# Kernel tuning notes

Measured on AMD Instinct MI355X. Metric: run time of the kernel, lower is better.

The kernel has to match this reference:

```python
import jax, jax.numpy as jnp
import numpy as np

B, S, D, F = 32, 512, 1024, 4096
R_COMMON, R_DOMAIN, E = 16, 16, 8
ALPHA = 2.0


def setup_inputs() -> dict:
    key = jax.random.key(0)
    ks = jax.random.split(key, 12)
    sd = lambda k, shape: jax.random.normal(k, shape, dtype=jnp.float32) * (1.0 / np.sqrt(shape[-1]))
    return {
        "hidden_states": jax.random.normal(ks[0], (B, S, D), dtype=jnp.float32),
        "expert_ids": jax.random.randint(ks[1], (B,), 0, E, dtype=jnp.int32),
        # nn.Linear weights: [out_features, in_features]
        "wi": sd(ks[2], (F, D)),
        "wo": sd(ks[3], (D, F)),
        "common_wi_a": sd(ks[4], (R_COMMON, D)),
        "common_wi_b": sd(ks[5], (F, R_COMMON)),
        "common_wo_a": sd(ks[6], (R_COMMON, F)),
        "common_wo_b": sd(ks[7], (D, R_COMMON)),
        # stacked per-expert LoRA weights
        "experts_wi_a": sd(ks[8], (E, R_DOMAIN, D)),
        "experts_wi_b": sd(ks[9], (F, R_DOMAIN)) * jnp.ones((E, 1, 1)) * 0.0 + sd(ks[9], (E, F, R_DOMAIN)),
        "experts_wo_a": sd(ks[10], (E, R_DOMAIN, F)),
        "experts_wo_b": sd(ks[11], (E, D, R_DOMAIN)),
    }


def _expert_lora(x, expert_ids, Wa, Wb):
    """Per-row (dim 0) expert LoRA correction, vectorized via gather.

    x: [B, S, din]; Wa: [E, r, din]; Wb: [E, dout, r].
    Equivalent to the per-expert mask-gather/scatter-add loop since each
    row belongs to exactly one expert.
    """
    Ab = Wa[expert_ids]  # [B, r, din]
    Bb = Wb[expert_ids]  # [B, dout, r]
    low = jnp.einsum("bsd,brd->bsr", x, Ab)
    return ALPHA * jnp.einsum("bsr,bor->bso", low, Bb)


def reference(hidden_states, expert_ids, wi, wo,
              common_wi_a, common_wi_b, common_wo_a, common_wo_b,
              experts_wi_a, experts_wi_b, experts_wo_a, experts_wo_b):
    x = hidden_states
    hidden_i = jnp.einsum("bsd,fd->bsf", x, wi)
    hidden_i += ALPHA * jnp.einsum("bsr,fr->bsf", jnp.einsum("bsd,rd->bsr", x, common_wi_a), common_wi_b)
    hidden_i += _expert_lora(x, expert_ids, experts_wi_a, experts_wi_b)
    hidden_i = jax.nn.relu(hidden_i)  # dense_act_fn='relu'; dropout is identity (eval)
    hidden_o = jnp.einsum("bsf,df->bsd", hidden_i, wo)
    hidden_o += ALPHA * jnp.einsum("bsr,dr->bsd", jnp.einsum("bsf,rf->bsr", hidden_i, common_wo_a), common_wo_b)
    hidden_o += _expert_lora(hidden_i, expert_ids, experts_wo_a, experts_wo_b)
    return hidden_o
```

## Files before the change

### kernel.cpp

```cpp
#include <hip/hip_runtime.h>
#include <hip/hip_bf16.h>
#include <stdint.h>

#define B_ 32
#define S_ 512
#define D_ 1024
#define F_ 4096
#define N_ (B_*S_)
#define E_ 8
#define ALPHA_ 2.0f

#define LDA1 1088
#define LDA2 4160

typedef __hip_bfloat16 bf16;
typedef __attribute__((ext_vector_type(8))) short short8;
typedef __attribute__((ext_vector_type(8))) __bf16 bf16x8;
typedef __attribute__((ext_vector_type(4))) float f32x4;

__device__ __forceinline__ f32x4 mfma_bf16(short8 a, short8 b, f32x4 c) {
    return __builtin_amdgcn_mfma_f32_16x16x32_bf16(
        __builtin_bit_cast(bf16x8, a), __builtin_bit_cast(bf16x8, b), c, 0, 0, 0);
}

__device__ __forceinline__ void gload_lds16(const void* g, void* l) {
    __builtin_amdgcn_global_load_lds((const __attribute__((address_space(1))) void*)g,
                                     (__attribute__((address_space(3))) void*)l, 16, 0, 0);
}

__device__ __forceinline__ unsigned pack2(float a, float b) {
    unsigned short x = __builtin_bit_cast(unsigned short, __float2bfloat16(a));
    unsigned short y = __builtin_bit_cast(unsigned short, __float2bfloat16(b));
    return (unsigned)x | ((unsigned)y << 16);
}
__device__ __forceinline__ uint2 pack4(float4 v) {
    return make_uint2(pack2(v.x, v.y), pack2(v.z, v.w));
}

__global__ __launch_bounds__(256) void prep_w_kernel(
    const float* __restrict__ wi, const float* __restrict__ wo,
    const float* __restrict__ cwia, const float* __restrict__ cwib,
    const float* __restrict__ cwoa, const float* __restrict__ cwob,
    const float* __restrict__ ewia, const float* __restrict__ ewib,
    const float* __restrict__ ewoa, const float* __restrict__ ewob,
    bf16* __restrict__ wi_b, bf16* __restrict__ wo_b,
    bf16* __restrict__ ex1, bf16* __restrict__ ex2,
    bf16* __restrict__ wilo, bf16* __restrict__ wolo)
{
    const int tid0 = blockIdx.x * blockDim.x + threadIdx.x;
    const int stride = gridDim.x * blockDim.x;

    for (int i = tid0; i < F_*D_/4; i += stride) {
        ((uint2*)wi_b)[i] = pack4(((const float4*)wi)[i]);
        ((uint2*)wo_b)[i] = pack4(((const float4*)wo)[i]);
    }
    for (int i = tid0; i < E_*F_*16; i += stride) {
        int e = i >> 16; int rem = i & 0xFFFF; int f = rem >> 4; int r = rem & 15;
        bf16* dst = ex1 + (((size_t)e*F_ + f) << 6);
        dst[r]      = __float2bfloat16(cwib[f*16 + r]);
        dst[16 + r] = __float2bfloat16(ewib[(((size_t)e*F_ + f) << 4) + r]);
        dst[32 + r] = __float2bfloat16(0.f);
        dst[48 + r] = __float2bfloat16(0.f);
    }
    for (int i = tid0; i < E_*D_*16; i += stride) {
        int e = i >> 14; int rem = i & 0x3FFF; int d = rem >> 4; int r = rem & 15;
        bf16* dst = ex2 + (((size_t)e*D_ + d) << 6);
        dst[r]      = __float2bfloat16(cwob[d*16 + r]);
        dst[16 + r] = __float2bfloat16(ewob[(((size_t)e*D_ + d) << 4) + r]);
        dst[32 + r] = __float2bfloat16(0.f);
        dst[48 + r] = __float2bfloat16(0.f);
    }
    for (int i = tid0; i < E_*32*(D_/4); i += stride) {
        int e = i / (32*(D_/4)); int rem = i - e*(32*(D_/4));
        int r = rem / (D_/4); int c4 = (rem % (D_/4)) * 4;
        const float* src = (r < 16) ? (cwia + (size_t)r*D_ + c4)
                                    : (ewia + ((size_t)(e*16 + (r-16)))*D_ + c4);
        *(uint2*)(wilo + ((size_t)(e*32 + r))*D_ + c4) = pack4(*(const float4*)src);
    }
    for (int i = tid0; i < E_*32*(F_/4); i += stride) {
        int e = i / (32*(F_/4)); int rem = i - e*(32*(F_/4));
        int r = rem / (F_/4); int c4 = (rem % (F_/4)) * 4;
        const float* src = (r < 16) ? (cwoa + (size_t)r*F_ + c4)
                                    : (ewoa + ((size_t)(e*16 + (r-16)))*F_ + c4);
        *(uint2*)(wolo + ((size_t)(e*32 + r))*F_ + c4) = pack4(*(const float4*)src);
    }
}

__global__ __launch_bounds__(256) void prep_x_kernel(
    const float* __restrict__ x, bf16* __restrict__ A1)
{
    const int tid0 = blockIdx.x * blockDim.x + threadIdx.x;
    const int stride = gridDim.x * blockDim.x;
    for (int i = tid0; i < N_*(D_/4); i += stride) {
        int row = i >> 8; int c4 = (i & 255) << 2;
        float4 v = *(const float4*)(x + (size_t)i * 4);
        *(uint2*)(A1 + (size_t)row*LDA1 + c4) = pack4(v);
    }
    for (int i = tid0; i < N_*8; i += stride) {
        int row = i >> 3; int c = (i & 7) << 2;
        *(uint2*)(A1 + (size_t)row*LDA1 + 1056 + c) = make_uint2(0u, 0u);
    }
}

template<int K>
__global__ __launch_bounds__(256) void lowproj_kernel(
    const bf16* __restrict__ A, const bf16* __restrict__ W,
    const int* __restrict__ eids, bf16* __restrict__ Out,
    int lda, int kout)
{
    constexpr int BM = 64, BK = 64;
    __shared__ __align__(16) bf16 Asm[BM*BK];
    __shared__ __align__(16) bf16 Wsm[32*BK];

    const int tid = threadIdx.x;
    const int row0 = blockIdx.x * BM;
    const int e = eids[row0 >> 9];
    const int w = tid >> 6, lane = tid & 63;
    const int tr = tid >> 3, ts = tid & 7;
    const int lrow = lane & 15;
    const int lk16 = (lane >> 4) << 4;

    f32x4 acc[2] = {};

    int aoff, woff[2];
    { int r = w*16 + lrow; aoff = r*128 + (lk16 ^ ((r & 7) << 4)); }
    #pragma unroll
    for (int n = 0; n < 2; ++n) {
        int r = n*16 + lrow; woff[n] = r*128 + (lk16 ^ ((r & 7) << 4));
    }
    const bf16* Wp = W + (size_t)e * 32 * K;

    #pragma unroll 1
    for (int kt = 0; kt < K/BK; ++kt) {
        const int k0 = kt * BK;
        #pragma unroll
        for (int i = 0; i < 2; ++i) {
            int row = tr + 32*i;
            int slot = ts ^ (row & 7);
            gload_lds16(A + (size_t)(row0 + row)*lda + k0 + slot*8,
                        (char*)Asm + row*128 + ts*16);
        }
        {
            int row = tr;
            int slot = ts ^ (row & 7);
            gload_lds16(Wp + (size_t)row*K + k0 + slot*8,
                        (char*)Wsm + row*128 + ts*16);
        }
        __syncthreads();
        #pragma unroll
        for (int kk = 0; kk < 2; ++kk) {
            short8 a = *(const short8*)((const char*)Asm + (aoff ^ (kk << 6)));
            #pragma unroll
            for (int n = 0; n < 2; ++n) {
                short8 b = *(const short8*)((const char*)Wsm + (woff[n] ^ (kk << 6)));
                acc[n] = mfma_bf16(a, b, acc[n]);
            }
        }
        __syncthreads();
    }

    const int jrow = (lane >> 4) << 2;
    #pragma unroll
    for (int n = 0; n < 2; ++n) {
        #pragma unroll
        for (int j = 0; j < 4; ++j) {
            int r = row0 + w*16 + jrow + j;
            int c = n*16 + lrow;
            Out[(size_t)r*lda + kout + c] = __float2bfloat16(ALPHA_ * acc[n][j]);
        }
    }
    #pragma unroll
    for (int i = 0; i < 8; ++i) {
        int idx = tid*8 + i;
        int r = idx >> 5, c = idx & 31;
        Out[(size_t)(row0 + r)*lda + kout + 32 + c] = __float2bfloat16(0.f);
    }
}

#define DSREAD(base, off) (*(const short8*)((const char*)(base) + (off)))

#define STAGE4(gptr, ld, ldsbase)                                          \
    _Pragma("unroll")                                                      \
    for (int i_ = 0; i_ < 4; ++i_) {                                       \
        int row_ = tr + 64*i_;                                             \
        int slot_ = ts ^ (row_ & 7);                                       \
        gload_lds16((gptr) + (size_t)row_*(ld) + slot_*8,                  \
                    (char*)(ldsbase) + row_*128 + ts*16);                  \
    }

#define STAGE_TILE(KTN, AL, BL)                                            \
  { STAGE4(Ag + (size_t)(KTN)*64, LDAe, AL);                               \
    if ((KTN) < KMAIN_EL/64) { STAGE4(Bg + (size_t)(KTN)*64, LDBe, BL); }  \
    else                     { STAGE4(Bxg, 64, BL); } }

#define TILE_BODY(AC, BC, DOSTAGE, AN, BN, KTN)                            \
  {                                                                        \
             \
    if (DOSTAGE) { STAGE_TILE((KTN), AN, BN); }                            \
    short8 af[4][2]; short8 bq[4][2];                                      \
                                     \
    _Pragma("unroll") for (int m = 0; m < 4; ++m)                          \
      _Pragma("unroll") for (int kk = 0; kk < 2; ++kk)                     \
        af[m][kk] = DSREAD(AC, aoff[m] ^ (kk << 6));                       \
    _Pragma("unroll") for (int n = 0; n < 2; ++n)                          \
      _Pragma("unroll") for (int kk = 0; kk < 2; ++kk)                     \
        bq[n][kk] = DSREAD(BC, boff[n] ^ (kk << 6));                       \
    __builtin_amdgcn_s_setprio(1);                                         \
    _Pragma("unroll") for (int m = 0; m < 4; ++m)                          \
      _Pragma("unroll") for (int n = 0; n < 2; ++n)                        \
        _Pragma("unroll") for (int kk = 0; kk < 2; ++kk)                   \
          acc[m][n] = mfma_bf16(af[m][kk], bq[n][kk], acc[m][n]);          \
    __builtin_amdgcn_s_setprio(0);                                         \
                                                   \
    _Pragma("unroll") for (int n = 2; n < 4; ++n)                          \
      _Pragma("unroll") for (int kk = 0; kk < 2; ++kk)                     \
        bq[n][kk] = DSREAD(BC, boff[n] ^ (kk << 6));                       \
    __builtin_amdgcn_s_setprio(1);                                         \
    _Pragma("unroll") for (int m = 0; m < 4; ++m)                          \
      _Pragma("unroll") for (int n = 2; n < 4; ++n)                        \
        _Pragma("unroll") for (int kk = 0; kk < 2; ++kk)                   \
          acc[m][n] = mfma_bf16(af[m][kk], bq[n][kk], acc[m][n]);          \
    __builtin_amdgcn_s_setprio(0);                                         \
                                              \
    _Pragma("unroll") for (int m = 0; m < 4; ++m)                          \
      _Pragma("unroll") for (int kk = 0; kk < 2; ++kk)                     \
        af[m][kk] = DSREAD(AC, aoff[m+4] ^ (kk << 6));                     \
    __builtin_amdgcn_s_setprio(1);                                         \
    _Pragma("unroll") for (int m = 0; m < 4; ++m)                          \
      _Pragma("unroll") for (int n = 0; n < 2; ++n)                        \
        _Pragma("unroll") for (int kk = 0; kk < 2; ++kk)                   \
          acc[m+4][n] = mfma_bf16(af[m][kk], bq[n][kk], acc[m+4][n]);      \
    __builtin_amdgcn_s_setprio(0);                                         \
                                                             \
    __builtin_amdgcn_s_setprio(1);                                         \
    _Pragma("unroll") for (int m = 0; m < 4; ++m)                          \
      _Pragma("unroll") for (int n = 2; n < 4; ++n)                        \
        _Pragma("unroll") for (int kk = 0; kk < 2; ++kk)                   \
          acc[m+4][n] = mfma_bf16(af[m][kk], bq[n][kk], acc[m+4][n]);      \
    __builtin_amdgcn_s_setprio(0);                                         \
    __syncthreads();                                                       \
  }

template<int KMAIN_EL, int LDAe, int LDBe, int LDCe, int NCOLSe, bool RELU_BF16>
__global__ __launch_bounds__(512, 2) void gemm256_kernel(
    const bf16* __restrict__ A, const bf16* __restrict__ Bmain,
    const bf16* __restrict__ Bextra, const int* __restrict__ eids,
    void* __restrict__ C)
{
    constexpr int MT = N_/256;
    constexpr int NT = NCOLSe/256;
    constexpr int NWG = MT*NT;
    constexpr int KTILES = KMAIN_EL/64 + 1;
    static_assert((KTILES & 1) == 1, "pair loop + tail assumes odd KTILES");
    static_assert(NWG % 8 == 0, "xcd swizzle needs nwg%8==0");
    constexpr int CPX = NWG/8;

    __shared__ __align__(16) bf16 As[2][256*64];
    __shared__ __align__(16) bf16 Bs[2][256*64];

    const int bid = blockIdx.x;
    const int wg = (bid & 7) * CPX + (bid >> 3);
    const int mt = wg % MT, nt = wg / MT;
    const int arow0 = mt * 256, bcol0 = nt * 256;
    const int e = eids[arow0 >> 9];

    const int tid = threadIdx.x;
    const int lane = tid & 63;
    const int wid = tid >> 6;
    const int wm = wid >> 2, wn = wid & 3;
    const int tr = tid >> 3, ts = tid & 7;

    const bf16* Ag  = A + (size_t)arow0 * LDAe;
    const bf16* Bg  = Bmain + (size_t)bcol0 * LDBe;
    const bf16* Bxg = Bextra + ((size_t)e * NCOLSe + bcol0) * 64;

    int aoff[8], boff[4];
    const int lk16 = (lane >> 4) << 4;
    #pragma unroll
    for (int m = 0; m < 8; ++m) {
        int r = wm*128 + m*16 + (lane & 15);
        aoff[m] = r*128 + (lk16 ^ ((r & 7) << 4));
    }
    #pragma unroll
    for (int n = 0; n < 4; ++n) {
        int r = wn*64 + n*16 + (lane & 15);
        boff[n] = r*128 + (lk16 ^ ((r & 7) << 4));
    }

    f32x4 acc[8][4] = {};

    STAGE_TILE(0, As[0], Bs[0]);
    __syncthreads();

    #pragma unroll 1
    for (int t = 0; t < KTILES - 1; t += 2) {
        TILE_BODY(As[0], Bs[0], true, As[1], Bs[1], t + 1);
        TILE_BODY(As[1], Bs[1], true, As[0], Bs[0], t + 2);
    }
    TILE_BODY(As[0], Bs[0], false, As[1], Bs[1], 0);

    const int jrow = (lane >> 4) << 2;
    if constexpr (RELU_BF16) {
        bf16* Cb = (bf16*)C;
        #pragma unroll
        for (int m = 0; m < 8; ++m)
            #pragma unroll
            for (int j = 0; j < 4; ++j) {
                size_t rbase = (size_t)(arow0 + wm*128 + m*16 + jrow + j) * LDCe;
                #pragma unroll
                for (int n = 0; n < 4; ++n) {
                    float v = acc[m][n][j];
                    v = v > 0.f ? v : 0.f;
                    Cb[rbase + bcol0 + wn*64 + n*16 + (lane & 15)] = __float2bfloat16(v);
                }
            }
    } else {
        float* Cf = (float*)C;
        #pragma unroll
        for (int m = 0; m < 8; ++m)
            #pragma unroll
            for (int j = 0; j < 4; ++j) {
                size_t rbase = (size_t)(arow0 + wm*128 + m*16 + jrow + j) * LDCe;
                #pragma unroll
                for (int n = 0; n < 4; ++n)
                    Cf[rbase + bcol0 + wn*64 + n*16 + (lane & 15)] = acc[m][n][j];
            }
    }
}

extern "C" void kernel_launch(void* const* d_in, const int* in_sizes, int n_in,
                              void* d_out, int out_size, void* d_ws, size_t ws_size,
                              hipStream_t stream)
{
    const float* x    = (const float*)d_in[0];
    const int*   eids = (const int*)d_in[1];
    const float* wi   = (const float*)d_in[2];
    const float* wo   = (const float*)d_in[3];
    const float* cwia = (const float*)d_in[4];
    const float* cwib = (const float*)d_in[5];
    const float* cwoa = (const float*)d_in[6];
    const float* cwob = (const float*)d_in[7];
    const float* ewia = (const float*)d_in[8];
    const float* ewib = (const float*)d_in[9];
    const float* ewoa = (const float*)d_in[10];
    const float* ewob = (const float*)d_in[11];

    char* p = (char*)d_ws;
    bf16* A1   = (bf16*)p; p += (size_t)N_*LDA1*sizeof(bf16);
    bf16* A2   = (bf16*)p; p += (size_t)N_*LDA2*sizeof(bf16);
    bf16* wi_b = (bf16*)p; p += (size_t)F_*D_*sizeof(bf16);
    bf16* wo_b = (bf16*)p; p += (size_t)D_*F_*sizeof(bf16);
    bf16* ex1  = (bf16*)p; p += (size_t)E_*F_*64*sizeof(bf16);
    bf16* ex2  = (bf16*)p; p += (size_t)E_*D_*64*sizeof(bf16);
    bf16* wilo = (bf16*)p; p += (size_t)E_*32*D_*sizeof(bf16);
    bf16* wolo = (bf16*)p; p += (size_t)E_*32*F_*sizeof(bf16);

    prep_w_kernel<<<dim3(512), dim3(256), 0, stream>>>(
        wi, wo, cwia, cwib, cwoa, cwob, ewia, ewib, ewoa, ewob,
        wi_b, wo_b, ex1, ex2, wilo, wolo);

    prep_x_kernel<<<dim3(2048), dim3(256), 0, stream>>>(x, A1);

    lowproj_kernel<D_><<<dim3(N_/64), dim3(256), 0, stream>>>(
        A1, wilo, eids, A1, LDA1, D_);

    gemm256_kernel<D_, LDA1, D_, LDA2, F_, true>
        <<<dim3((N_/256)*(F_/256)), dim3(512), 0, stream>>>(A1, wi_b, ex1, eids, A2);

    lowproj_kernel<F_><<<dim3(N_/64), dim3(256), 0, stream>>>(
        A2, wolo, eids, A2, LDA2, F_);

    gemm256_kernel<F_, LDA2, F_, D_, D_, false>
        <<<dim3((N_/256)*(D_/256)), dim3(512), 0, stream>>>(A2, wo_b, ex2, eids, d_out);

    (void)in_sizes; (void)n_in; (void)out_size; (void)ws_size;
}
```

Baseline: 529.1 us.

## Split tile staging into halves interleaved with MFMA phases using partial vmcnt waits

Restructures the double-buffered GEMM main loop so global-to-LDS loads for the next tile are issued in quarter chunks between MFMA groups. Full __syncthreads is replaced with raw s_barrier plus explicit s_waitcnt vmcnt(N) so loads stay in flight across barriers. The goal is to spread memory issue across the tile and avoid a full drain each iteration. It relies on hand-counted vmcnt values and on barrier placement being correct for the LDS buffer reuse, so a miscount risks data races.

```diff
diff --git a/kernel.cpp b/kernel.cpp
--- a/kernel.cpp
+++ b/kernel.cpp
@@ -178,67 +178,73 @@
 }
 
 #define DSREAD(base, off) (*(const short8*)((const char*)(base) + (off)))
-
-#define STAGE4(gptr, ld, ldsbase)                                          \
-    _Pragma("unroll")                                                      \
-    for (int i_ = 0; i_ < 4; ++i_) {                                       \
-        int row_ = tr + 64*i_;                                             \
-        int slot_ = ts ^ (row_ & 7);                                       \
-        gload_lds16((gptr) + (size_t)row_*(ld) + slot_*8,                  \
-                    (char*)(ldsbase) + row_*128 + ts*16);                  \
-    }
-
-#define STAGE_TILE(KTN, AL, BL)                                            \
-  { STAGE4(Ag + (size_t)(KTN)*64, LDAe, AL);                               \
-    if ((KTN) < KMAIN_EL/64) { STAGE4(Bg + (size_t)(KTN)*64, LDBe, BL); }  \
-    else                     { STAGE4(Bxg, 64, BL); } }
-
-#define TILE_BODY(AC, BC, DOSTAGE, AN, BN, KTN)                            \
+#define VMW4 asm volatile("s_waitcnt vmcnt(4)" ::: "memory")
+#define VMW2 asm volatile("s_waitcnt vmcnt(2)" ::: "memory")
+#define VMW0 asm volatile("s_waitcnt vmcnt(0)" ::: "memory")
+#define VMNONE (void)0
+#define BAR __builtin_amdgcn_s_barrier()
+
+#define STAGE_A_HALF(KTN, AL, h)                                           \
+  { const bf16* gpA_ = Ag + (size_t)(KTN)*64;                              \
+    int rA_ = tr + 64*(h);                                                 \
+    int sA_ = ts ^ (rA_ & 7);                                              \
+    gload_lds16(gpA_ + (size_t)rA_*LDAe + sA_*8,                           \
+                (char*)(AL) + rA_*128 + ts*16);                            \
+    int rA2_ = rA_ + 128;                                                  \
+    gload_lds16(gpA_ + (size_t)rA2_*LDAe + sA_*8,                          \
+                (char*)(AL) + rA2_*128 + ts*16); }
+
+#define STAGE_B_HALF(KTN, BL, h)                                           \
+  { const bf16* gpB_; int bldB_; int bkB_;                                 \
+    if ((KTN) < KMAIN_EL/64) { gpB_ = Bg; bldB_ = LDBe; bkB_ = (KTN)*64; } \
+    else                     { gpB_ = Bxg; bldB_ = 64; bkB_ = 0; }         \
+    int rB_ = (tr & 31) + 64*(tr >> 5) + 32*(h);                           \
+    int sB_ = ts ^ (rB_ & 7);                                              \
+    gload_lds16(gpB_ + (size_t)rB_*bldB_ + bkB_ + sB_*8,                   \
+                (char*)(BL) + rB_*128 + ts*16);                            \
+    int rB2_ = rB_ + 128;                                                  \
+    gload_lds16(gpB_ + (size_t)rB2_*bldB_ + bkB_ + sB_*8,                  \
+                (char*)(BL) + rB2_*128 + ts*16); }
+
+#define RD_AF(dst, AC, base)                                               \
+  _Pragma("unroll") for (int m_ = 0; m_ < 4; ++m_)                         \
+    _Pragma("unroll") for (int k_ = 0; k_ < 2; ++k_)                       \
+      dst[m_][k_] = DSREAD(AC, aoff[(base)+m_] ^ (k_ << 6));
+
+#define RD_BQ(dst, BC, base)                                               \
+  _Pragma("unroll") for (int n_ = 0; n_ < 2; ++n_)                         \
+    _Pragma("unroll") for (int k_ = 0; k_ < 2; ++k_)                       \
+      dst[n_][k_] = DSREAD(BC, boff[(base)+n_] ^ (k_ << 6));
+
+#define MFMA16(afr, bqr, mb, nb)                                           \
+  __builtin_amdgcn_s_setprio(1);                                           \
+  _Pragma("unroll") for (int m_ = 0; m_ < 4; ++m_)                         \
+    _Pragma("unroll") for (int n_ = 0; n_ < 2; ++n_)                       \
+      _Pragma("unroll") for (int k_ = 0; k_ < 2; ++k_)                     \
+        acc[(mb)+m_][(nb)+n_] =                                            \
+            mfma_bf16(afr[m_][k_], bqr[n_][k_], acc[(mb)+m_][(nb)+n_]);    \
+  __builtin_amdgcn_s_setprio(0);
+
+#define TILE8(AC, BC, DOSTAGE, AN, BN, KTN, W1, W2, W4)                    \
   {                                                                        \
-             \
-    if (DOSTAGE) { STAGE_TILE((KTN), AN, BN); }                            \
-    short8 af[4][2]; short8 bq[4][2];                                      \
-                                     \
-    _Pragma("unroll") for (int m = 0; m < 4; ++m)                          \
-      _Pragma("unroll") for (int kk = 0; kk < 2; ++kk)                     \
-        af[m][kk] = DSREAD(AC, aoff[m] ^ (kk << 6));                       \
-    _Pragma("unroll") for (int n = 0; n < 2; ++n)                          \
-      _Pragma("unroll") for (int kk = 0; kk < 2; ++kk)                     \
-        bq[n][kk] = DSREAD(BC, boff[n] ^ (kk << 6));                       \
-    __builtin_amdgcn_s_setprio(1);                                         \
-    _Pragma("unroll") for (int m = 0; m < 4; ++m)                          \
-      _Pragma("unroll") for (int n = 0; n < 2; ++n)                        \
-        _Pragma("unroll") for (int kk = 0; kk < 2; ++kk)                   \
-          acc[m][n] = mfma_bf16(af[m][kk], bq[n][kk], acc[m][n]);          \
-    __builtin_amdgcn_s_setprio(0);                                         \
-                                                   \
-    _Pragma("unroll") for (int n = 2; n < 4; ++n)                          \
-      _Pragma("unroll") for (int kk = 0; kk < 2; ++kk)                     \
-        bq[n][kk] = DSREAD(BC, boff[n] ^ (kk << 6));                       \
-    __builtin_amdgcn_s_setprio(1);                                         \
-    _Pragma("unroll") for (int m = 0; m < 4; ++m)                          \
-      _Pragma("unroll") for (int n = 2; n < 4; ++n)                        \
-        _Pragma("unroll") for (int kk = 0; kk < 2; ++kk)                   \
-          acc[m][n] = mfma_bf16(af[m][kk], bq[n][kk], acc[m][n]);          \
-    __builtin_amdgcn_s_setprio(0);                                         \
-                                              \
-    _Pragma("unroll") for (int m = 0; m < 4; ++m)                          \
-      _Pragma("unroll") for (int kk = 0; kk < 2; ++kk)                     \
-        af[m][kk] = DSREAD(AC, aoff[m+4] ^ (kk << 6));                     \
-    __builtin_amdgcn_s_setprio(1);                                         \
-    _Pragma("unroll") for (int m = 0; m < 4; ++m)                          \
-      _Pragma("unroll") for (int n = 0; n < 2; ++n)                        \
-        _Pragma("unroll") for (int kk = 0; kk < 2; ++kk)                   \
-          acc[m+4][n] = mfma_bf16(af[m][kk], bq[n][kk], acc[m+4][n]);      \
-    __builtin_amdgcn_s_setprio(0);                                         \
-                                                             \
-    __builtin_amdgcn_s_setprio(1);                                         \
-    _Pragma("unroll") for (int m = 0; m < 4; ++m)                          \
-      _Pragma("unroll") for (int n = 2; n < 4; ++n)                        \
-        _Pragma("unroll") for (int kk = 0; kk < 2; ++kk)                   \
-          acc[m+4][n] = mfma_bf16(af[m][kk], bq[n][kk], acc[m+4][n]);      \
-    __builtin_amdgcn_s_setprio(0);                                         \
-    __syncthreads();                                                       \
+    short8 afl[4][2], afh[4][2], bql[2][2], bqh[2][2];                     \
+                         \
+    RD_AF(afl, AC, 0); RD_BQ(bql, BC, 0);                                  \
+    if (DOSTAGE) { STAGE_A_HALF(KTN, AN, 0); }                             \
+    W1; BAR;                                                               \
+    MFMA16(afl, bql, 0, 0);                                                \
+                                                                  \
+    RD_BQ(bqh, BC, 2);                                                     \
+    if (DOSTAGE) { STAGE_B_HALF(KTN, BN, 0); }                             \
+    W2; BAR;                                                               \
+    MFMA16(afl, bqh, 0, 2);                                                \
+                                                              \
+    RD_AF(afh, AC, 4);                                                     \
+    if (DOSTAGE) { STAGE_B_HALF(KTN, BN, 1); }                             \
+    MFMA16(afh, bql, 4, 0);                                                \
+    if (DOSTAGE) { STAGE_A_HALF(KTN, AN, 1); }                             \
+    W4; BAR;                                                               \
+    MFMA16(afh, bqh, 4, 2);                                                \
   }
 
 template<int KMAIN_EL, int LDAe, int LDBe, int LDCe, int NCOLSe, bool RELU_BF16>
@@ -289,15 +295,18 @@
 
     f32x4 acc[8][4] = {};
 
-    STAGE_TILE(0, As[0], Bs[0]);
-    __syncthreads();
+    STAGE_A_HALF(0, As[0], 0);
+    STAGE_B_HALF(0, Bs[0], 0);
+    STAGE_B_HALF(0, Bs[0], 1);
+    STAGE_A_HALF(0, As[0], 1);
+    VMW4; BAR;
 
     #pragma unroll 1
     for (int t = 0; t < KTILES - 1; t += 2) {
-        TILE_BODY(As[0], Bs[0], true, As[1], Bs[1], t + 1);
-        TILE_BODY(As[1], Bs[1], true, As[0], Bs[0], t + 2);
-    }
-    TILE_BODY(As[0], Bs[0], false, As[1], Bs[1], 0);
+        TILE8(As[0], Bs[0], true, As[1], Bs[1], t + 1, VMW4, VMW4, VMW4);
+        TILE8(As[1], Bs[1], true, As[0], Bs[0], t + 2, VMW4, VMW4, VMW4);
+    }
+    TILE8(As[0], Bs[0], false, As[1], Bs[1], 0, VMW2, VMW0, VMNONE);
 
     const int jrow = (lane >> 4) << 2;
     if constexpr (RELU_BF16) {
```

After: 471.1 us. 1.12x faster.
